# Kernel tuning notes

Measured on AMD Instinct MI355X. Metric: run time of the kernel, lower is better.

The kernel has to match this reference:

```python
import jax, jax.numpy as jnp
from jax import lax
import numpy as np

# dims
N_DIA, DLEN = 48, 64            # 48 dialogues, 64 utterances each
N = N_DIA * DLEN                # total utterances = 3072
D = 512                         # n_dim (modal feature dim)
H = 512                         # nhidden
NL = 2                          # GCNII layers
NS = 2                          # n_speakers
ALPHA, LAMDA = 0.1, 0.5
PI = float(np.pi)
SCALE = 0.99999                 # acos clamp factor from original code


def setup_inputs() -> dict:
    key = jax.random.key(0)
    ks = jax.random.split(key, 8)
    a = jax.random.normal(ks[0], (N, D), jnp.float32)
    v = jax.random.normal(ks[1], (N, D), jnp.float32)
    l = jax.random.normal(ks[2], (N, D), jnp.float32)
    qmask = jax.random.uniform(ks[3], (DLEN, N_DIA, NS), jnp.float32)
    dia_len = np.full((N_DIA,), DLEN, dtype=np.int64)  # static segment lengths
    # learned params
    W_spk = 0.02 * jax.random.normal(ks[4], (NS, D), jnp.float32)      # speaker_embeddings
    W0 = jax.random.normal(ks[5], (D, H), jnp.float32) / np.sqrt(D)    # graph_net.fcs[0]
    b0 = jnp.zeros((H,), jnp.float32)
    Wg = jax.random.normal(ks[6], (NL, H, H), jnp.float32) / np.sqrt(H)  # GCNII conv weights
    return {"a": a, "v": v, "l": l, "qmask": qmask, "dia_len": dia_len,
            "W_spk": W_spk, "W0": W0, "b0": b0, "Wg": Wg}


def _angular_sim(cs):
    # 1 - acos(cs*0.99999)/pi, clipped for numerical safety of acos
    return 1.0 - jnp.arccos(jnp.clip(cs * SCALE, -SCALE, SCALE)) / PI


def _build_adj(feats, seg_mask):
    # feats: list of 3 arrays [N, D]; seg_mask: [N, N] same-dialogue block mask
    n = feats[0].shape[0]
    normed = [f * jax.lax.rsqrt(jnp.sum(f * f, axis=1, keepdims=True)) for f in feats]
    adj = jnp.zeros((3 * n, 3 * n), feats[0].dtype)
    ar = jnp.arange(n)
    for m in range(3):
        for nn_ in range(3):
            if m == nn_:
                # within-modality: block-diagonal (per dialogue) angular cosine similarity
                sim = _angular_sim(normed[m] @ normed[m].T) * seg_mask
                adj = adj.at[m * n:(m + 1) * n, nn_ * n:(nn_ + 1) * n].set(sim)
            else:
                # cross-modality: only diagonal (same utterance) entries
                cs = jnp.sum(normed[m] * normed[nn_], axis=1)
                adj = adj.at[m * n + ar, nn_ * n + ar].set(_angular_sim(cs))
    # symmetric degree normalization D^-1/2 A D^-1/2
    dinv = jax.lax.rsqrt(adj.sum(axis=1))
    return adj * dinv[:, None] * dinv[None, :]


def reference(a, v, l, qmask, dia_len, W_spk, W0, b0, Wg):
    dl = np.asarray(dia_len)
    nb = dl.shape[0]
    # node -> (position-in-dialogue, dialogue-id), static from dia_len
    dia_id = np.repeat(np.arange(nb), dl)
    pos = np.concatenate([np.arange(x) for x in dl])
    qflat = qmask[pos, dia_id]                 # [N, NS], matches torch.cat order
    spk_idx = jnp.argmax(qflat, axis=-1)       # [N]
    l = l + W_spk[spk_idx]                     # use_speaker=True, 'l' in modals

    seg = jnp.asarray(dia_id)
    seg_mask = (seg[:, None] == seg[None, :]).astype(a.dtype)  # [N, N]
    adj = _build_adj([a, v, l], seg_mask)      # [3N, 3N]

    x = jnp.concatenate([a, v, l], axis=0)     # [3N, D]
    # GCNII_lyc (eval mode: dropout is identity)
    h0 = jax.nn.relu(x @ W0 + b0)              # [3N, H]
    thetas = jnp.log(LAMDA / jnp.arange(1, NL + 1, dtype=x.dtype) + 1.0)

    def step(h, wt):
        W, theta = wt
        hi = adj @ h
        support = (1.0 - ALPHA) * hi + ALPHA * h0   # variant=False
        h = jax.nn.relu(theta * (support @ W) + (1.0 - theta) * support)
        return h, None

    h, _ = lax.scan(step, h0, (Wg, thetas))
    feat = jnp.concatenate([x, h], axis=-1)    # use_residue=True -> [3N, D+H]
    n = a.shape[0]
    # regroup per-utterance modal features: [N, 3*(D+H)]
    out = jnp.concatenate([feat[:n], feat[n:2 * n], feat[2 * n:3 * n]], axis=-1)
    return out
```

## Files before the change

kernel.cpp:

```cpp
#include <hip/hip_runtime.h>
#include <math.h>

#define N_DIA 48
#define NTOT  3072
#define DD    512
#define M3    9216
#define SEG   ((size_t)NTOT * DD)

#define SCALE_F 0.99999f
#define PI_F    3.14159274101257324f

typedef __attribute__((ext_vector_type(8))) short frag8;
typedef __attribute__((ext_vector_type(4))) float f32x4;

__device__ __forceinline__ float ang_sim(float cs) {
    float cc = cs * SCALE_F;
    cc = fminf(fmaxf(cc, -SCALE_F), SCALE_F);
    return 1.0f - acosf(cc) / PI_F;
}
__device__ __forceinline__ unsigned short f2bf(float x) {
    union { float f; unsigned int u; } c; c.f = x;
    unsigned int r = c.u + 0x7fffu + ((c.u >> 16) & 1u);
    return (unsigned short)(r >> 16);
}
__device__ __forceinline__ float bf2f(unsigned short h) {
    union { unsigned int u; float f; } c; c.u = ((unsigned int)h) << 16;
    return c.f;
}
__device__ __forceinline__ void gload16(const unsigned short* g, unsigned short* s) {
    __builtin_amdgcn_global_load_lds(
        (const __attribute__((address_space(1))) unsigned int*)g,
        (__attribute__((address_space(3))) unsigned int*)s, 16, 0, 0);
}

__global__ __launch_bounds__(64) void k_pre(
    const float* __restrict__ a, const float* __restrict__ v,
    const float* __restrict__ l, const float* __restrict__ qmask,
    const float* __restrict__ Wspk,
    float* __restrict__ out, unsigned short* __restrict__ xb,
    float* __restrict__ invn, float* __restrict__ cross)
{
    int i = blockIdx.x, t = threadIdx.x;
    int pos = i & 63, dia = i >> 6;
    int qb = (pos * N_DIA + dia) * 2;
    float q0 = qmask[qb], q1 = qmask[qb + 1];
    int spk = (q0 >= q1) ? 0 : 1;
    const float4* av4 = (const float4*)(a + (size_t)i * DD);
    const float4* vv4 = (const float4*)(v + (size_t)i * DD);
    const float4* lv4 = (const float4*)(l + (size_t)i * DD);
    const float4* wv4 = (const float4*)(Wspk + (size_t)spk * DD);
    float* ob = out + (size_t)i * 3072;
    float saa = 0, svv = 0, sll = 0, sav = 0, sal = 0, svl = 0;
#pragma unroll
    for (int e = 0; e < 2; e++) {
        int idx = t * 2 + e;
        float4 xa = av4[idx], xv = vv4[idx], xd = lv4[idx], xw = wv4[idx];
        float4 xL = make_float4(xd.x + xw.x, xd.y + xw.y, xd.z + xw.z, xd.w + xw.w);
        *(float4*)(ob + idx * 4)        = xa;
        *(float4*)(ob + 1024 + idx * 4) = xv;
        *(float4*)(ob + 2048 + idx * 4) = xL;
        ushort4 ya, yv, yl;
        ya.x = f2bf(xa.x); ya.y = f2bf(xa.y); ya.z = f2bf(xa.z); ya.w = f2bf(xa.w);
        yv.x = f2bf(xv.x); yv.y = f2bf(xv.y); yv.z = f2bf(xv.z); yv.w = f2bf(xv.w);
        yl.x = f2bf(xL.x); yl.y = f2bf(xL.y); yl.z = f2bf(xL.z); yl.w = f2bf(xL.w);
        *(ushort4*)(xb + (size_t)i * DD + idx * 4) = ya;
        *(ushort4*)(xb + SEG + (size_t)i * DD + idx * 4) = yv;
        *(ushort4*)(xb + 2 * SEG + (size_t)i * DD + idx * 4) = yl;
        saa += xa.x * xa.x + xa.y * xa.y + xa.z * xa.z + xa.w * xa.w;
        svv += xv.x * xv.x + xv.y * xv.y + xv.z * xv.z + xv.w * xv.w;
        sll += xL.x * xL.x + xL.y * xL.y + xL.z * xL.z + xL.w * xL.w;
        sav += xa.x * xv.x + xa.y * xv.y + xa.z * xv.z + xa.w * xv.w;
        sal += xa.x * xL.x + xa.y * xL.y + xa.z * xL.z + xa.w * xL.w;
        svl += xv.x * xL.x + xv.y * xL.y + xv.z * xL.z + xv.w * xL.w;
    }
#pragma unroll
    for (int off = 32; off; off >>= 1) {
        saa += __shfl_down(saa, off, 64);
        svv += __shfl_down(svv, off, 64);
        sll += __shfl_down(sll, off, 64);
        sav += __shfl_down(sav, off, 64);
        sal += __shfl_down(sal, off, 64);
        svl += __shfl_down(svl, off, 64);
    }
    if (t == 0) {
        float ina = 1.0f / sqrtf(saa);
        float inv_ = 1.0f / sqrtf(svv);
        float inl = 1.0f / sqrtf(sll);
        invn[i] = ina; invn[NTOT + i] = inv_; invn[2 * NTOT + i] = inl;
        cross[i]            = ang_sim(sav * ina * inv_);
        cross[NTOT + i]     = ang_sim(sal * ina * inl);
        cross[2 * NTOT + i] = ang_sim(svl * inv_ * inl);
    }
}

__global__ __launch_bounds__(256) void k_gram_mfma(
    const unsigned short* __restrict__ xb, const float* __restrict__ invn,
    const float* __restrict__ cross, float* __restrict__ blk,
    float* __restrict__ dinv)
{
    __shared__ __align__(16) unsigned short Xs[16 * 2048];
    int d = blockIdx.x, m = blockIdx.y;
    int t = threadIdx.x;
    int lane = t & 63, wv = t >> 6;
    int mrow = m * NTOT + d * 64;
    const unsigned short* src = xb + (size_t)mrow * DD;
#pragma unroll
    for (int c = 0; c < 16; c++) {
        gload16(src + (size_t)(t >> 2) * DD + c * 32 + (t & 3) * 8,
                &Xs[c * 2048 + wv * 512]);
    }
    __syncthreads();

    int rsel = lane & 15, quad = lane >> 4;
    f32x4 acc[4];
#pragma unroll
    for (int j = 0; j < 4; j++) acc[j] = (f32x4){0.f, 0.f, 0.f, 0.f};
#pragma unroll
    for (int c = 0; c < 16; c++) {
        const unsigned short* base = &Xs[c * 2048];
        frag8 bf[4];
#pragma unroll
        for (int j = 0; j < 4; j++)
            bf[j] = *(const frag8*)&base[(j * 16 + rsel) * 32 + quad * 8];
        frag8 af = *(const frag8*)&base[(wv * 16 + rsel) * 32 + quad * 8];
#pragma unroll
        for (int j = 0; j < 4; j++)
            acc[j] = __builtin_amdgcn_mfma_f32_16x16x32_bf16(af, bf[j], acc[j], 0, 0, 0);
    }

    size_t bbase = (size_t)(m * N_DIA + d) * 4096;
    int rowl0 = wv * 16 + quad * 4;
    float ir[4], rs[4] = {0.f, 0.f, 0.f, 0.f};
#pragma unroll
    for (int r = 0; r < 4; r++) ir[r] = invn[mrow + rowl0 + r];
#pragma unroll
    for (int j = 0; j < 4; j++) {
        int coll = j * 16 + rsel;
        float ic = invn[mrow + coll];
#pragma unroll
        for (int r = 0; r < 4; r++) {
            float sim = ang_sim(acc[j][r] * ir[r] * ic);
            blk[bbase + (size_t)(rowl0 + r) * 64 + coll] = sim;
            rs[r] += sim;
        }
    }
#pragma unroll
    for (int off = 8; off; off >>= 1)
#pragma unroll
        for (int r = 0; r < 4; r++) rs[r] += __shfl_down(rs[r], off, 16);
    if (rsel == 0) {
#pragma unroll
        for (int r = 0; r < 4; r++) {
            int gi = d * 64 + rowl0 + r;
            float c1, c2;
            if (m == 0)      { c1 = cross[gi];        c2 = cross[NTOT + gi]; }
            else if (m == 1) { c1 = cross[gi];        c2 = cross[2 * NTOT + gi]; }
            else             { c1 = cross[NTOT + gi]; c2 = cross[2 * NTOT + gi]; }
            dinv[m * NTOT + gi] = 1.0f / sqrtf(rs[r] + c1 + c2);
        }
    }
}

__global__ void k_wt(const float* __restrict__ W0, const float* __restrict__ Wg,
                     unsigned short* __restrict__ Wt) {
    __shared__ float tile[32][33];
    int bx = blockIdx.x, by = blockIdx.y, mm = blockIdx.z;
    const float* W = (mm == 0) ? W0 : Wg + (size_t)(mm - 1) * DD * DD;
    int t = threadIdx.x;
    int tx = t & 31, ty = t >> 5;
#pragma unroll
    for (int q = 0; q < 4; q++) {
        int k = by * 32 + ty + q * 8;
        tile[ty + q * 8][tx] = W[(size_t)k * DD + bx * 32 + tx];
    }
    __syncthreads();
#pragma unroll
    for (int q = 0; q < 4; q++) {
        int n = bx * 32 + ty + q * 8;
        Wt[(size_t)mm * DD * DD + (size_t)n * DD + by * 32 + tx] = f2bf(tile[tx][ty + q * 8]);
    }
}

__global__ __launch_bounds__(256) void k_gemm_mfma(
    const unsigned short* __restrict__ A, const unsigned short* __restrict__ Wt,
    const float* __restrict__ bias, const unsigned short* __restrict__ resid,
    float* __restrict__ outp, float theta, int mode)
{
    __shared__ __align__(16) unsigned short As[64 * 32];
    __shared__ __align__(16) unsigned short Bs[128 * 32];
    int t = threadIdx.x;
    int lane = t & 63, wv = t >> 6;
    int mbase = blockIdx.y * 64, nbase = blockIdx.x * 128;
    int srow = lane >> 2;
    int scol = (lane & 3) * 8;
    int rsel = lane & 15, quad = lane >> 4;

    const unsigned short* Ag  = A  + (size_t)(mbase + wv * 16 + srow) * DD + scol;
    const unsigned short* Bg0 = Wt + (size_t)(nbase + wv * 32 + srow) * DD + scol;
    const unsigned short* Bg1 = Wt + (size_t)(nbase + wv * 32 + 16 + srow) * DD + scol;
    unsigned short* Asl  = &As[wv * 512];
    unsigned short* Bsl0 = &Bs[wv * 1024];
    unsigned short* Bsl1 = &Bs[wv * 1024 + 512];

    f32x4 acc[8];
#pragma unroll
    for (int i = 0; i < 8; i++) acc[i] = (f32x4){0.f, 0.f, 0.f, 0.f};

    for (int kt = 0; kt < DD; kt += 32) {
        __syncthreads();
        gload16(Ag + kt, Asl);
        gload16(Bg0 + kt, Bsl0);
        gload16(Bg1 + kt, Bsl1);
        __syncthreads();
        frag8 af[4], bfr[2];
#pragma unroll
        for (int i = 0; i < 4; i++)
            af[i] = *(const frag8*)&As[(i * 16 + rsel) * 32 + quad * 8];
#pragma unroll
        for (int j = 0; j < 2; j++)
            bfr[j] = *(const frag8*)&Bs[(wv * 32 + j * 16 + rsel) * 32 + quad * 8];
#pragma unroll
        for (int i = 0; i < 4; i++)
#pragma unroll
            for (int j = 0; j < 2; j++)
                acc[i * 2 + j] = __builtin_amdgcn_mfma_f32_16x16x32_bf16(
                    af[i], bfr[j], acc[i * 2 + j], 0, 0, 0);
    }

    float omt = 1.0f - theta;
    int mq = mbase / NTOT;
    int iu0 = mbase - mq * NTOT;
#pragma unroll
    for (int i = 0; i < 4; i++)
#pragma unroll
        for (int j = 0; j < 2; j++) {
            int col = nbase + wv * 32 + j * 16 + rsel;
            int rowl = i * 16 + quad * 4;
            f32x4 r = acc[i * 2 + j];
#pragma unroll
            for (int rr = 0; rr < 4; rr++) {
                float vv = r[rr];
                int row = mbase + rowl + rr;
                size_t o = (size_t)row * DD + col;
                if (mode == 0) vv += bias[col];
                else vv = theta * vv + omt * bf2f(resid[o]);
                vv = fmaxf(vv, 0.f);
                if (mode == 2)
                    outp[(size_t)(iu0 + rowl + rr) * 3072 + mq * 1024 + 512 + col] = vv;
                else
                    outp[o] = vv;
            }
        }
}

__global__ __launch_bounds__(256) void k_adjmul(
    const float* __restrict__ blk, const float* __restrict__ cross,
    const float* __restrict__ dinv, const float* __restrict__ h,
    const float* __restrict__ h0, unsigned short* __restrict__ supb) {
    __shared__ float Ab[64][65];
    __shared__ float4 hs[64][32];
    int cc = blockIdx.x;
    int d = blockIdx.y, m = blockIdx.z;
    int dbase = d * 64, cb = cc * 128;
    int t = threadIdx.x;
    size_t bbase = (size_t)(m * N_DIA + d) * 4096;
#pragma unroll
    for (int q = 0; q < 16; q++) {
        int e = t + 256 * q;
        int i = e >> 6, j = e & 63;
        Ab[i][j] = blk[bbase + e] * dinv[m * NTOT + dbase + i] * dinv[m * NTOT + dbase + j];
    }
#pragma unroll
    for (int q = 0; q < 8; q++) {
        int f4 = t + 256 * q;
        int j = f4 >> 5, c4 = f4 & 31;
        hs[j][c4] = *(const float4*)(h + (size_t)(m * NTOT + dbase + j) * DD + cb + c4 * 4);
    }
    __syncthreads();
    int tx = t & 31, ty = t >> 5;
    float4 acc[8];
#pragma unroll
    for (int i = 0; i < 8; i++) acc[i] = make_float4(0.f, 0.f, 0.f, 0.f);
    for (int j = 0; j < 64; j++) {
        float4 b = hs[j][tx];
#pragma unroll
        for (int rr = 0; rr < 8; rr++) {
            float aw = Ab[ty * 8 + rr][j];
            acc[rr].x += aw * b.x; acc[rr].y += aw * b.y;
            acc[rr].z += aw * b.z; acc[rr].w += aw * b.w;
        }
    }
#pragma unroll
    for (int rr = 0; rr < 8; rr++) {
        int i = ty * 8 + rr;
        int gi = dbase + i;
        float dm = dinv[m * NTOT + gi];
#pragma unroll
        for (int n = 0; n < 3; n++) {
            if (n == m) continue;
            int p = m + n - 1;
            float cval = cross[p * NTOT + gi] * dm * dinv[n * NTOT + gi];
            float4 hv = *(const float4*)(h + (size_t)(n * NTOT + gi) * DD + cb + tx * 4);
            acc[rr].x += cval * hv.x; acc[rr].y += cval * hv.y;
            acc[rr].z += cval * hv.z; acc[rr].w += cval * hv.w;
        }
        size_t o = (size_t)(m * NTOT + gi) * DD + cb + tx * 4;
        float4 h0v = *(const float4*)(h0 + o);
        ushort4 w;
        w.x = f2bf(0.9f * acc[rr].x + 0.1f * h0v.x);
        w.y = f2bf(0.9f * acc[rr].y + 0.1f * h0v.y);
        w.z = f2bf(0.9f * acc[rr].z + 0.1f * h0v.z);
        w.w = f2bf(0.9f * acc[rr].w + 0.1f * h0v.w);
        *(ushort4*)(supb + o) = w;
    }
}

extern "C" void kernel_launch(void* const* d_in, const int* in_sizes, int n_in,
                              void* d_out, int out_size, void* d_ws, size_t ws_size,
                              hipStream_t stream) {
    (void)in_sizes; (void)n_in; (void)out_size; (void)ws_size;
    const float* a     = (const float*)d_in[0];
    const float* v     = (const float*)d_in[1];
    const float* l     = (const float*)d_in[2];
    const float* qmask = (const float*)d_in[3];
    const float* Wspk  = (const float*)d_in[5];
    const float* W0    = (const float*)d_in[6];
    const float* b0    = (const float*)d_in[7];
    const float* Wg    = (const float*)d_in[8];
    float* out = (float*)d_out;
    float* ws = (float*)d_ws;

    const size_t big = 3 * SEG;
    float* invn  = ws;
    float* blk   = invn + M3;
    float* cross = blk + (size_t)3 * N_DIA * 4096;
    float* dinvp = cross + M3;
    unsigned short* Wt  = (unsigned short*)(dinvp + M3);
    unsigned short* xb  = (unsigned short*)((float*)Wt + 393216);
    unsigned short* supb = xb;
    float* h0 = (float*)(xb + big);
    float* h  = h0 + big;

    k_pre<<<NTOT, 64, 0, stream>>>(a, v, l, qmask, Wspk, out, xb, invn, cross);
    k_wt <<<dim3(16, 16, 3), 256, 0, stream>>>(W0, Wg, Wt);
    k_gram_mfma<<<dim3(N_DIA, 3), 256, 0, stream>>>(xb, invn, cross, blk, dinvp);

    const float th1 = 0.40546510810816438f;
    const float th2 = 0.22314355131420976f;

    k_gemm_mfma<<<dim3(4, 144), 256, 0, stream>>>(xb, Wt, b0, xb, h0, 0.f, 0);
    k_adjmul<<<dim3(4, N_DIA, 3), 256, 0, stream>>>(blk, cross, dinvp, h0, h0, supb);
    k_gemm_mfma<<<dim3(4, 144), 256, 0, stream>>>(supb, Wt + (size_t)DD * DD, b0, supb, h, th1, 1);
    k_adjmul<<<dim3(4, N_DIA, 3), 256, 0, stream>>>(blk, cross, dinvp, h, h0, supb);
    k_gemm_mfma<<<dim3(4, 144), 256, 0, stream>>>(supb, Wt + (size_t)2 * DD * DD, b0, supb, out, th2, 2);
}
```

Baseline: 212.9 us.

## Move adjacency multiply onto bf16 MFMA with transposed bf16 hidden states

The per-dialogue adjacency-times-hidden multiply now runs on MFMA bf16 instructions instead of fp32 FMAs. To feed it, the GEMM epilogue writes hidden states in bf16 twice, once transposed and once row-major, replacing the fp32 row-major output. The bf16 storage roughly halves intermediate memory traffic but adds a strided transposed store and further rounding of h and h0.

```diff
diff --git a/kernel.cpp b/kernel.cpp
--- a/kernel.cpp
+++ b/kernel.cpp
@@ -184,7 +184,8 @@
 __global__ __launch_bounds__(256) void k_gemm_mfma(
     const unsigned short* __restrict__ A, const unsigned short* __restrict__ Wt,
     const float* __restrict__ bias, const unsigned short* __restrict__ resid,
-    float* __restrict__ outp, float theta, int mode)
+    unsigned short* __restrict__ outT, unsigned short* __restrict__ outR,
+    float* __restrict__ outF, float theta, int mode)
 {
     __shared__ __align__(16) unsigned short As[64 * 32];
     __shared__ __align__(16) unsigned short Bs[128 * 32];
@@ -236,82 +237,121 @@
         for (int j = 0; j < 2; j++) {
             int col = nbase + wv * 32 + j * 16 + rsel;
             int rowl = i * 16 + quad * 4;
+            int rowb = mbase + rowl;
             f32x4 r = acc[i * 2 + j];
+            float vv[4];
 #pragma unroll
             for (int rr = 0; rr < 4; rr++) {
-                float vv = r[rr];
-                int row = mbase + rowl + rr;
-                size_t o = (size_t)row * DD + col;
-                if (mode == 0) vv += bias[col];
-                else vv = theta * vv + omt * bf2f(resid[o]);
-                vv = fmaxf(vv, 0.f);
-                if (mode == 2)
-                    outp[(size_t)(iu0 + rowl + rr) * 3072 + mq * 1024 + 512 + col] = vv;
-                else
-                    outp[o] = vv;
+                float x = r[rr];
+                if (mode == 0) x += bias[col];
+                else x = theta * x + omt * bf2f(resid[(size_t)(rowb + rr) * DD + col]);
+                vv[rr] = fmaxf(x, 0.f);
+            }
+            if (mode == 2) {
+#pragma unroll
+                for (int rr = 0; rr < 4; rr++)
+                    outF[(size_t)(iu0 + rowl + rr) * 3072 + mq * 1024 + 512 + col] = vv[rr];
+            } else {
+                ushort4 w4;
+                w4.x = f2bf(vv[0]); w4.y = f2bf(vv[1]);
+                w4.z = f2bf(vv[2]); w4.w = f2bf(vv[3]);
+                *(ushort4*)(outT + (size_t)col * M3 + rowb) = w4;
+#pragma unroll
+                for (int rr = 0; rr < 4; rr++)
+                    outR[(size_t)(rowb + rr) * DD + col] = f2bf(vv[rr]);
             }
         }
 }
 
-__global__ __launch_bounds__(256) void k_adjmul(
+__global__ __launch_bounds__(256) void k_adjmul_mfma(
     const float* __restrict__ blk, const float* __restrict__ cross,
-    const float* __restrict__ dinv, const float* __restrict__ h,
-    const float* __restrict__ h0, unsigned short* __restrict__ supb) {
-    __shared__ float Ab[64][65];
-    __shared__ float4 hs[64][32];
-    int cc = blockIdx.x;
-    int d = blockIdx.y, m = blockIdx.z;
-    int dbase = d * 64, cb = cc * 128;
+    const float* __restrict__ dinv,
+    const unsigned short* __restrict__ hT, const unsigned short* __restrict__ hrow,
+    const unsigned short* __restrict__ h0row, unsigned short* __restrict__ supb)
+{
+    __shared__ __align__(16) unsigned short AdL[64 * 72];
+    __shared__ __align__(16) unsigned short hTL[256 * 72];
+    __shared__ float dv[64];
+    int cc = blockIdx.x, d = blockIdx.y, m = blockIdx.z;
     int t = threadIdx.x;
+    int lane = t & 63, wv = t >> 6;
+    int dbase = d * 64, cbase = cc * 256;
+    int rsel = lane & 15, quad = lane >> 4;
+
+    if (t < 64) dv[t] = dinv[m * NTOT + dbase + t];
+    __syncthreads();
+
     size_t bbase = (size_t)(m * N_DIA + d) * 4096;
 #pragma unroll
-    for (int q = 0; q < 16; q++) {
-        int e = t + 256 * q;
-        int i = e >> 6, j = e & 63;
-        Ab[i][j] = blk[bbase + e] * dinv[m * NTOT + dbase + i] * dinv[m * NTOT + dbase + j];
-    }
-#pragma unroll
-    for (int q = 0; q < 8; q++) {
-        int f4 = t + 256 * q;
-        int j = f4 >> 5, c4 = f4 & 31;
-        hs[j][c4] = *(const float4*)(h + (size_t)(m * NTOT + dbase + j) * DD + cb + c4 * 4);
+    for (int q = 0; q < 4; q++) {
+        int e4 = t + 256 * q;
+        int i = e4 >> 4, j4 = e4 & 15;
+        float4 w = *(const float4*)(blk + bbase + (size_t)i * 64 + j4 * 4);
+        float di = dv[i];
+        ushort4 o;
+        o.x = f2bf(w.x * di * dv[j4 * 4 + 0]);
+        o.y = f2bf(w.y * di * dv[j4 * 4 + 1]);
+        o.z = f2bf(w.z * di * dv[j4 * 4 + 2]);
+        o.w = f2bf(w.w * di * dv[j4 * 4 + 3]);
+        *(ushort4*)&AdL[i * 72 + j4 * 4] = o;
+    }
+#pragma unroll
+    for (int p = 0; p < 8; p++) {
+        int e = t + 256 * p;
+        int cl = e >> 3;
+        int jo = (e & 7) * 8;
+        uint4 w = *(const uint4*)(hT + (size_t)(cbase + cl) * M3 + m * NTOT + dbase + jo);
+        *(uint4*)&hTL[cl * 72 + jo] = w;
     }
     __syncthreads();
-    int tx = t & 31, ty = t >> 5;
-    float4 acc[8];
-#pragma unroll
-    for (int i = 0; i < 8; i++) acc[i] = make_float4(0.f, 0.f, 0.f, 0.f);
-    for (int j = 0; j < 64; j++) {
-        float4 b = hs[j][tx];
-#pragma unroll
-        for (int rr = 0; rr < 8; rr++) {
-            float aw = Ab[ty * 8 + rr][j];
-            acc[rr].x += aw * b.x; acc[rr].y += aw * b.y;
-            acc[rr].z += aw * b.z; acc[rr].w += aw * b.w;
+
+    f32x4 acc[16];
+#pragma unroll
+    for (int i = 0; i < 16; i++) acc[i] = (f32x4){0.f, 0.f, 0.f, 0.f};
+#pragma unroll
+    for (int kk = 0; kk < 2; kk++) {
+        frag8 bfr[4];
+#pragma unroll
+        for (int it = 0; it < 4; it++)
+            bfr[it] = *(const frag8*)&AdL[(it * 16 + rsel) * 72 + kk * 32 + quad * 8];
+#pragma unroll
+        for (int jc = 0; jc < 4; jc++) {
+            frag8 af = *(const frag8*)&hTL[(wv * 64 + jc * 16 + rsel) * 72 + kk * 32 + quad * 8];
+#pragma unroll
+            for (int it = 0; it < 4; it++)
+                acc[jc * 4 + it] = __builtin_amdgcn_mfma_f32_16x16x32_bf16(
+                    af, bfr[it], acc[jc * 4 + it], 0, 0, 0);
         }
     }
-#pragma unroll
-    for (int rr = 0; rr < 8; rr++) {
-        int i = ty * 8 + rr;
-        int gi = dbase + i;
-        float dm = dinv[m * NTOT + gi];
-#pragma unroll
-        for (int n = 0; n < 3; n++) {
-            if (n == m) continue;
-            int p = m + n - 1;
-            float cval = cross[p * NTOT + gi] * dm * dinv[n * NTOT + gi];
-            float4 hv = *(const float4*)(h + (size_t)(n * NTOT + gi) * DD + cb + tx * 4);
-            acc[rr].x += cval * hv.x; acc[rr].y += cval * hv.y;
-            acc[rr].z += cval * hv.z; acc[rr].w += cval * hv.w;
+
+    int n1, n2, p1, p2;
+    if (m == 0)      { n1 = 1; n2 = 2; p1 = 0; p2 = 1; }
+    else if (m == 1) { n1 = 0; n2 = 2; p1 = 0; p2 = 2; }
+    else             { n1 = 0; n2 = 1; p1 = 1; p2 = 2; }
+#pragma unroll
+    for (int it = 0; it < 4; it++) {
+        int il = it * 16 + rsel;
+        int gi = dbase + il;
+        float dm = dv[il];
+        float cv1 = cross[p1 * NTOT + gi] * dm * dinv[n1 * NTOT + gi];
+        float cv2 = cross[p2 * NTOT + gi] * dm * dinv[n2 * NTOT + gi];
+        size_t r1 = (size_t)(n1 * NTOT + gi) * DD;
+        size_t r2 = (size_t)(n2 * NTOT + gi) * DD;
+        size_t r0 = (size_t)(m * NTOT + gi) * DD;
+#pragma unroll
+        for (int jc = 0; jc < 4; jc++) {
+            int cb = cbase + wv * 64 + jc * 16 + quad * 4;
+            ushort4 u1 = *(const ushort4*)(hrow + r1 + cb);
+            ushort4 u2 = *(const ushort4*)(hrow + r2 + cb);
+            ushort4 u0 = *(const ushort4*)(h0row + r0 + cb);
+            f32x4 aa = acc[jc * 4 + it];
+            ushort4 w;
+            w.x = f2bf(0.9f * (aa[0] + cv1 * bf2f(u1.x) + cv2 * bf2f(u2.x)) + 0.1f * bf2f(u0.x));
+            w.y = f2bf(0.9f * (aa[1] + cv1 * bf2f(u1.y) + cv2 * bf2f(u2.y)) + 0.1f * bf2f(u0.y));
+            w.z = f2bf(0.9f * (aa[2] + cv1 * bf2f(u1.z) + cv2 * bf2f(u2.z)) + 0.1f * bf2f(u0.z));
+            w.w = f2bf(0.9f * (aa[3] + cv1 * bf2f(u1.w) + cv2 * bf2f(u2.w)) + 0.1f * bf2f(u0.w));
+            *(ushort4*)(supb + r0 + cb) = w;
         }
-        size_t o = (size_t)(m * NTOT + gi) * DD + cb + tx * 4;
-        float4 h0v = *(const float4*)(h0 + o);
-        ushort4 w;
-        w.x = f2bf(0.9f * acc[rr].x + 0.1f * h0v.x);
-        w.y = f2bf(0.9f * acc[rr].y + 0.1f * h0v.y);
-        w.z = f2bf(0.9f * acc[rr].z + 0.1f * h0v.z);
-        w.w = f2bf(0.9f * acc[rr].w + 0.1f * h0v.w);
-        *(ushort4*)(supb + o) = w;
     }
 }
 
@@ -330,16 +370,17 @@
     float* out = (float*)d_out;
     float* ws = (float*)d_ws;
 
-    const size_t big = 3 * SEG;
     float* invn  = ws;
     float* blk   = invn + M3;
     float* cross = blk + (size_t)3 * N_DIA * 4096;
     float* dinvp = cross + M3;
     unsigned short* Wt  = (unsigned short*)(dinvp + M3);
-    unsigned short* xb  = (unsigned short*)((float*)Wt + 393216);
+    unsigned short* xb  = Wt + (size_t)3 * DD * DD;
     unsigned short* supb = xb;
-    float* h0 = (float*)(xb + big);
-    float* h  = h0 + big;
+    unsigned short* h0T = xb + 3 * SEG;
+    unsigned short* h0r = h0T + 3 * SEG;
+    unsigned short* h1T = h0r + 3 * SEG;
+    unsigned short* h1r = h1T + 3 * SEG;
 
     k_pre<<<NTOT, 64, 0, stream>>>(a, v, l, qmask, Wspk, out, xb, invn, cross);
     k_wt <<<dim3(16, 16, 3), 256, 0, stream>>>(W0, Wg, Wt);
@@ -348,9 +389,14 @@
     const float th1 = 0.40546510810816438f;
     const float th2 = 0.22314355131420976f;
 
-    k_gemm_mfma<<<dim3(4, 144), 256, 0, stream>>>(xb, Wt, b0, xb, h0, 0.f, 0);
-    k_adjmul<<<dim3(4, N_DIA, 3), 256, 0, stream>>>(blk, cross, dinvp, h0, h0, supb);
-    k_gemm_mfma<<<dim3(4, 144), 256, 0, stream>>>(supb, Wt + (size_t)DD * DD, b0, supb, h, th1, 1);
-    k_adjmul<<<dim3(4, N_DIA, 3), 256, 0, stream>>>(blk, cross, dinvp, h, h0, supb);
-    k_gemm_mfma<<<dim3(4, 144), 256, 0, stream>>>(supb, Wt + (size_t)2 * DD * DD, b0, supb, out, th2, 2);
-}
+    k_gemm_mfma<<<dim3(4, 144), 256, 0, stream>>>(xb, Wt, b0, nullptr,
+                                                  h0T, h0r, nullptr, 0.f, 0);
+    k_adjmul_mfma<<<dim3(2, N_DIA, 3), 256, 0, stream>>>(blk, cross, dinvp,
+                                                         h0T, h0r, h0r, supb);
+    k_gemm_mfma<<<dim3(4, 144), 256, 0, stream>>>(supb, Wt + (size_t)DD * DD, nullptr, supb,
+                                                  h1T, h1r, nullptr, th1, 1);
+    k_adjmul_mfma<<<dim3(2, N_DIA, 3), 256, 0, stream>>>(blk, cross, dinvp,
+                                                         h1T, h1r, h0r, supb);
+    k_gemm_mfma<<<dim3(4, 144), 256, 0, stream>>>(supb, Wt + (size_t)2 * DD * DD, nullptr, supb,
+                                                  nullptr, nullptr, out, th2, 2);
+}
```

Result: faster. 202.6 us (-4.9%).
